# Performance work log

Hardware: AMD Instinct MI355X
Metric: run time of the kernel (lower is better)

Reference implementation:

```python
import jax, jax.numpy as jnp
import numpy as np

R_MAX = 4.0   # CUTOFF_RADIUS
N_RBF = 16    # N_BASIS
DEPTH = 2
C = 64        # pp/pi/ii node width


def setup_inputs() -> dict:
    key = jax.random.key(0)
    ks = jax.random.split(key, 16)
    N, P, B = 10000, 100000, 512
    Z = jax.random.randint(ks[0], (N,), 0, 100, dtype=jnp.int32)
    # displacement vectors; scaled so distances spread over (0, ~5) around the 4A cutoff
    pair_diff = jax.random.normal(ks[1], (P, 3), jnp.float32) * 1.5
    pair_i = jax.random.randint(ks[2], (P,), 0, N, dtype=jnp.int32)
    pair_j = jax.random.randint(ks[3], (P,), 0, N, dtype=jnp.int32)
    atom_batch = jnp.sort(jax.random.randint(ks[4], (N,), 0, B, dtype=jnp.int32))

    def w(k, shape, fan_in):
        return (jax.random.normal(k, shape, jnp.float32) / np.float32(np.sqrt(fan_in)))

    params = dict(
        embed_w=w(ks[5], (100, C), 1.0),                      # atom-type embedding
        pp_w1=w(ks[6], (DEPTH, C, C), C), pp_b1=jnp.zeros((DEPTH, C), jnp.float32),
        pp_w2=w(ks[7], (DEPTH, C, C), C), pp_b2=jnp.zeros((DEPTH, C), jnp.float32),
        pi_w1=w(ks[8], (DEPTH, 2 * C, C), 2 * C), pi_b1=jnp.zeros((DEPTH, C), jnp.float32),
        pi_w2=w(ks[9], (DEPTH, C, C * N_RBF), C), pi_b2=jnp.zeros((DEPTH, C * N_RBF), jnp.float32),
        ii_w1=w(ks[10], (DEPTH, C, C), C),                    # ii layers are bias-free
        ii_w2=w(ks[11], (DEPTH, C, 3 * C), C),                # output split 3-ways (p1/p3-scale/diff)
        pix_w=w(ks[12], (DEPTH, C, C), C),                    # equivariant (bias-free) p3 mix
        ro_w1=w(ks[13], (C, 32), C), ro_b1=jnp.zeros((32,), jnp.float32),
        ro_w2=w(ks[14], (32, 1), 32), ro_b2=jnp.zeros((1,), jnp.float32),
    )
    return dict(Z=Z, pair_diff=pair_diff, pair_i=pair_i, pair_j=pair_j,
                atom_batch=atom_batch, n_mol=B, **params)


def reference(Z, pair_diff, pair_i, pair_j, atom_batch, n_mol,
              embed_w, pp_w1, pp_b1, pp_w2, pp_b2,
              pi_w1, pi_b1, pi_w2, pi_b2,
              ii_w1, ii_w2, pix_w,
              ro_w1, ro_b1, ro_w2, ro_b2):
    N = Z.shape[0]
    dist = jnp.sqrt(jnp.sum(pair_diff * pair_diff, axis=-1) + 1e-12)   # [P]
    dhat = pair_diff / dist[:, None]                                    # unit directions [P,3]

    # Gaussian RBF basis modulated by cosine cutoff
    centers = jnp.linspace(0.0, R_MAX, N_RBF, dtype=dist.dtype)
    sigma = R_MAX / (N_RBF - 1)
    rbf = jnp.exp(-0.5 * ((dist[:, None] - centers) / sigma) ** 2)      # [P,16]
    fc = 0.5 * (jnp.cos(jnp.pi * dist / R_MAX) + 1.0) * (dist < R_MAX)
    basis = rbf * fc[:, None]                                           # [P,16]

    p1 = embed_w[Z]                                  # scalar features [N,64]
    p3 = jnp.zeros((N, 3, C), p1.dtype)              # vector features [N,3,64]

    for d in range(DEPTH):
        # pp: atomwise MLP on scalars
        h = jnp.tanh(p1 @ pp_w1[d] + pp_b1[d])
        h = jnp.tanh(h @ pp_w2[d] + pp_b2[d])
        # pi: pairwise interaction modulated by radial basis
        pij = jnp.concatenate([h[pair_i], h[pair_j]], axis=-1)          # [P,128]
        g = jnp.tanh(pij @ pi_w1[d] + pi_b1[d])
        g = jnp.tanh(g @ pi_w2[d] + pi_b2[d]).reshape(-1, C, N_RBF)     # [P,64,16]
        i1 = jnp.einsum('pcb,pb->pc', g, basis)                         # [P,64]
        # ii: bias-free pair MLP, output split into three 64-channel blocks
        ii = jnp.tanh(i1 @ ii_w1[d]) @ ii_w2[d]                         # [P,192]
        i1a, i1b, i1c = jnp.split(ii, 3, axis=-1)
        # equivariant vector messages: gathered p3_j scaled + direction term
        p3j = jnp.einsum('pxc,cd->pxd', p3[pair_j], pix_w[d])           # [P,3,64]
        i3 = p3j * i1b[:, None, :] + dhat[:, :, None] * i1c[:, None, :]
        # ip: scatter-sum messages back to atoms, residual update
        p1 = p1 + jax.ops.segment_sum(i1a, pair_i, num_segments=N)
        p3 = p3 + jax.ops.segment_sum(i3, pair_i, num_segments=N)

    # Batchwise energy readout: atomwise MLP [64,32,1], sum over atom_batch
    h = jnp.tanh(p1 @ ro_w1 + ro_b1)
    atom_e = (h @ ro_w2 + ro_b2)[:, 0]                                  # [N]
    delta_energy = jax.ops.segment_sum(atom_e, atom_batch, num_segments=n_mol)
    return delta_energy
```

## Files before the change

kernel.cpp:

```cpp
#include <hip/hip_runtime.h>
#include <hip/hip_bf16.h>

#define PI_F 3.14159265358979323846f
#define TWO_LOG2E 2.885390081777927f

#define WWIN 5
#define NBUCK 12

typedef __bf16 bf16x8 __attribute__((ext_vector_type(8)));
typedef float  f32x4  __attribute__((ext_vector_type(4)));

#define MFMA16(a, b, c) __builtin_amdgcn_mfma_f32_16x16x32_bf16((a), (b), (c), 0, 0, 0)

__device__ __forceinline__ float fast_tanh(float x) {
    float e = __builtin_amdgcn_exp2f(TWO_LOG2E * x);
    return 1.0f - 2.0f * __fdividef(1.0f, e + 1.0f);
}

__global__ void k_setup(const int* __restrict__ Z,
                        const float* __restrict__ embed_w,
                        const float* __restrict__ pair_diff,
                        const float* __restrict__ pp_w1,
                        const float* __restrict__ pp_w2,
                        const float* __restrict__ pi_w1,
                        const float* __restrict__ pi_w2,
                        const float* __restrict__ ii_w1,
                        const float* __restrict__ ii_w2,
                        const float* __restrict__ pi_b2,
                        __bf16* __restrict__ ppbf,
                        __bf16* __restrict__ w2bf,
                        __bf16* __restrict__ w3bf,
                        __bf16* __restrict__ w4bf,
                        float* __restrict__ b2t,
                        float* __restrict__ p1,
                        int* __restrict__ pb0, int* __restrict__ hist,
                        float* __restrict__ out_f,
                        int N, int P, int out_size) {
    __shared__ int h[16];
    const int t = threadIdx.x;
    const int idx = blockIdx.x * 256 + t;

    if (t < 16) h[t] = 0;
    __syncthreads();
    if (idx < P) {
        float x = pair_diff[3 * idx + 0];
        float y = pair_diff[3 * idx + 1];
        float z = pair_diff[3 * idx + 2];
        float d = sqrtf(x * x + y * y + z * z + 1e-12f);
        int b0 = -1;
        if (d < 4.0f) {
            b0 = (int)floorf(d * 3.75f + 0.5f) - 2;
            b0 = min(NBUCK - 1, max(0, b0));
            atomicAdd(&h[b0], 1);
        }
        pb0[idx] = b0;
    }
    __syncthreads();
    if (t < 16 && blockIdx.x * 256 < P) hist[blockIdx.x * 16 + t] = h[t];

    if (idx < N * 64) {
        int n = idx >> 6, c = idx & 63;
        p1[idx] = embed_w[Z[n] * 64 + c];
    }

    if (idx < out_size) out_f[idx] = 0.f;

    if (idx < 32768) {
        int k = idx & 63;
        int o = (idx >> 6) & 63;
        int d = (idx >> 12) & 1;
        int m = idx >> 13;
        float val = 0.f;
        switch (m) {
            case 0: val = pp_w1[d * 4096 + k * 64 + o]; break;
            case 1: val = pp_w2[d * 4096 + k * 64 + o]; break;
            case 2: val = pi_w1[d * 8192 + k * 64 + o]; break;
            case 3: val = pi_w1[d * 8192 + (64 + k) * 64 + o]; break;
        }
        ppbf[idx] = (__bf16)val;
    } else if (idx < 182272) {
        int j = idx - 32768;
        if (j < 131072) {
            int d = j >> 16, r = j & 65535;
            int np = r >> 6, k = r & 63;
            int b = np >> 6, c = np & 63;
            w2bf[j] = (__bf16)pi_w2[d * 65536 + k * 1024 + c * 16 + b];
        } else if (j < 139264) {
            int tt = j - 131072;
            int d = tt >> 12, r = tt & 4095;
            int n = r >> 6, k = r & 63;
            w3bf[tt] = (__bf16)ii_w1[d * 4096 + k * 64 + n];
        } else if (j < 147456) {
            int tt = j - 139264;
            int d = tt >> 12, r = tt & 4095;
            int n = r >> 6, k = r & 63;
            w4bf[tt] = (__bf16)ii_w2[d * 12288 + k * 192 + n];
        } else if (j < 149504) {
            int tt = j - 147456;
            int d = tt >> 10, r = tt & 1023;
            int b = r >> 6, c = r & 63;
            b2t[tt] = pi_b2[d * 1024 + c * 16 + b];
        }
    }
}

__global__ void k_scan(const int* __restrict__ hist, int NBL, int NB,
                       int* __restrict__ meta, int* __restrict__ bases,
                       int* __restrict__ blk_b0, int* __restrict__ aiw) {
    __shared__ int tot[NBUCK];
    __shared__ int smeta[NBUCK + 1];
    __shared__ int stile[NBUCK + 1];
    const int t = threadIdx.x;
    const int b = t >> 6, lane = t & 63;
    if (b < NBUCK) {
        int run = 0;
        for (int base = 0; base < NBL; base += 64) {
            int blk = base + lane;
            int v = (blk < NBL) ? hist[blk * 16 + b] : 0;
            int x = v;
            #pragma unroll
            for (int off = 1; off < 64; off <<= 1) {
                int y = __shfl_up(x, off);
                if (lane >= off) x += y;
            }
            if (blk < NBL) bases[b * NBL + blk] = run + x - v;
            run += __shfl(x, 63);
        }
        if (lane == 0) tot[b] = run;
    }
    __syncthreads();
    if (t == 0) {
        int s = 0, tile = 0;
        #pragma unroll
        for (int bb = 0; bb < NBUCK; ++bb) {
            smeta[bb] = s;
            stile[bb] = tile;
            int ntile = (tot[bb] + 63) >> 6;
            s += ntile << 6;
            tile += ntile;
        }
        smeta[NBUCK] = s;
        stile[NBUCK] = tile;
    }
    __syncthreads();
    if (t < NBUCK + 1) meta[t] = smeta[t];
    if (b < NBUCK) {
        int pos = smeta[b] + tot[b] + lane;
        if (pos < smeta[b + 1]) aiw[pos] = -1;
    }
    for (int tile = t; tile < NB; tile += blockDim.x) {
        int bb = -1;
        #pragma unroll
        for (int k = 0; k < NBUCK; ++k)
            if (tile >= stile[k] && tile < stile[k + 1]) bb = k;
        blk_b0[tile] = bb;
    }
}

__global__ void k_scatter(const float* __restrict__ pair_diff,
                          const int* __restrict__ pair_i, const int* __restrict__ pair_j,
                          const int* __restrict__ pb0, const int* __restrict__ meta,
                          const int* __restrict__ bases, int NBL,
                          int* __restrict__ aiw, int* __restrict__ ajw,
                          float* __restrict__ basisw, int P) {
    __shared__ int wcnt[4][NBUCK];
    int t = threadIdx.x;
    int wv = t >> 6, lane = t & 63;
    if (t < 4 * NBUCK) ((int*)wcnt)[t] = 0;
    __syncthreads();
    int p = blockIdx.x * 256 + t;
    int b0 = (p < P) ? pb0[p] : -1;
    int rank = 0;
    unsigned long long lt = (lane == 63) ? 0x7FFFFFFFFFFFFFFFull
                                         : ((1ull << lane) - 1ull);
    #pragma unroll
    for (int b = 0; b < NBUCK; ++b) {
        unsigned long long m = __ballot(b0 == b);
        if (b0 == b) {
            rank = __popcll(m & lt);
            if (rank == 0) wcnt[wv][b] = __popcll(m);
        }
    }
    __syncthreads();
    if (b0 < 0) return;
    int local = rank;
    #pragma unroll
    for (int w = 0; w < 3; ++w)
        if (w < wv) local += wcnt[w][b0];
    int pos = meta[b0] + bases[b0 * NBL + blockIdx.x] + local;
    aiw[pos] = pair_i[p];
    ajw[pos] = pair_j[p];
    float x = pair_diff[3 * p + 0];
    float y = pair_diff[3 * p + 1];
    float z = pair_diff[3 * p + 2];
    float d = sqrtf(x * x + y * y + z * z + 1e-12f);
    float fc = 0.5f * (__cosf(PI_F * d * 0.25f) + 1.0f);
    float* bw = basisw + (size_t)pos * 8;
    #pragma unroll
    for (int wb = 0; wb < WWIN; ++wb) {
        float tt = (d - (float)(b0 + wb) * (4.0f / 15.0f)) * 3.75f;
        bw[wb] = __expf(-0.5f * tt * tt) * fc;
    }
    bw[5] = 0.f;
    bw[6] = 0.f;
    bw[7] = 0.f;
}

__device__ __forceinline__ void mfma_gemm64(const __bf16 (*S)[72], const __bf16* __restrict__ W,
                                            int ll, int lg, int wv, f32x4 acc[4], float init) {
    const f32x4 i4 = {init, init, init, init};
    #pragma unroll
    for (int mt = 0; mt < 4; ++mt) acc[mt] = i4;
    #pragma unroll
    for (int kt = 0; kt < 2; ++kt) {
        bf16x8 bw = *(const bf16x8*)(W + (size_t)(wv * 16 + ll) * 64 + kt * 32 + lg * 8);
        #pragma unroll
        for (int mt = 0; mt < 4; ++mt) {
            bf16x8 af = *(const bf16x8*)&S[mt * 16 + ll][kt * 32 + lg * 8];
            acc[mt] = MFMA16(af, bw, acc[mt]);
        }
    }
}

__launch_bounds__(256)
__global__ void k_pp(const float* __restrict__ p1,
                     const __bf16* __restrict__ w1bf, const float* __restrict__ b1,
                     const __bf16* __restrict__ w2bfp, const float* __restrict__ b2,
                     const __bf16* __restrict__ wubf, const __bf16* __restrict__ wvbf,
                     const float* __restrict__ bu,
                     float* __restrict__ u, float* __restrict__ v, int N) {
    __shared__ __bf16 sA[64][72];
    __shared__ __bf16 sH[64][72];
    const int t = threadIdx.x;
    const int a0 = blockIdx.x * 64;

    {
        int r = t >> 2, q = t & 3;
        int a = a0 + r;
        int cc = q * 16;
        bf16x8 x0, x1;
        if (a < N) {
            const f32x4* pp = (const f32x4*)(p1 + (size_t)a * 64 + cc);
            f32x4 p0 = pp[0], p1v = pp[1], p2 = pp[2], p3 = pp[3];
            #pragma unroll
            for (int e = 0; e < 4; ++e) {
                x0[e]     = (__bf16)p0[e];
                x0[4 + e] = (__bf16)p1v[e];
                x1[e]     = (__bf16)p2[e];
                x1[4 + e] = (__bf16)p3[e];
            }
        } else {
            #pragma unroll
            for (int e = 0; e < 8; ++e) { x0[e] = (__bf16)0.f; x1[e] = (__bf16)0.f; }
        }
        *(bf16x8*)&sA[r][cc]     = x0;
        *(bf16x8*)&sA[r][cc + 8] = x1;
    }
    __syncthreads();

    const int l  = t & 63;
    const int wv = t >> 6;
    const int ll = l & 15;
    const int lg = l >> 4;

    f32x4 acc[4];
    mfma_gemm64(sA, w1bf, ll, lg, wv, acc, b1[wv * 16 + ll]);
    #pragma unroll
    for (int mt = 0; mt < 4; ++mt)
        #pragma unroll
        for (int r = 0; r < 4; ++r)
            sH[mt * 16 + lg * 4 + r][wv * 16 + ll] = (__bf16)fast_tanh(acc[mt][r]);
    __syncthreads();
    mfma_gemm64(sH, w2bfp, ll, lg, wv, acc, b2[wv * 16 + ll]);
    #pragma unroll
    for (int mt = 0; mt < 4; ++mt)
        #pragma unroll
        for (int r = 0; r < 4; ++r)
            sA[mt * 16 + lg * 4 + r][wv * 16 + ll] = (__bf16)fast_tanh(acc[mt][r]);
    __syncthreads();
    f32x4 accV[4];
    mfma_gemm64(sA, wubf, ll, lg, wv, acc, bu[wv * 16 + ll]);
    mfma_gemm64(sA, wvbf, ll, lg, wv, accV, 0.f);
    #pragma unroll
    for (int mt = 0; mt < 4; ++mt) {
        #pragma unroll
        for (int r = 0; r < 4; ++r) {
            int a = a0 + mt * 16 + lg * 4 + r;
            if (a < N) {
                u[(size_t)a * 64 + wv * 16 + ll] = acc[mt][r];
                v[(size_t)a * 64 + wv * 16 + ll] = accV[mt][r];
            }
        }
    }
}

__launch_bounds__(256, 5)
__global__ void k_pair(const float* __restrict__ u, const float* __restrict__ v,
                       const int* __restrict__ aiw, const int* __restrict__ ajw,
                       const float* __restrict__ basisw,
                       const __bf16* __restrict__ w2bf, const float* __restrict__ b2t,
                       const __bf16* __restrict__ w3bf, const __bf16* __restrict__ w4bf,
                       const int* __restrict__ blk_b0,
                       float* __restrict__ p1) {
    __shared__ __bf16 sGH[64][72];
    __shared__ __bf16 sI1[64][72];
    __shared__ float sB[64][12];
    __shared__ int sPi[64];

    const int b0 = blk_b0[blockIdx.x];
    if (b0 < 0) return;
    const int blk64 = blockIdx.x * 64;

    const int t  = threadIdx.x;
    const int l  = t & 63;
    const int wv = t >> 6;
    const int ll = l & 15;
    const int lg = l >> 4;

    const __bf16* abase = w2bf + ((size_t)(b0 * 64 + wv * 16 + ll) << 6) + lg * 8;
    bf16x8 a0 = *(const bf16x8*)(abase);
    bf16x8 a1 = *(const bf16x8*)(abase + 32);

    {
        int r = t >> 2, q = t & 3;
        int p = blk64 + r;
        int ai = aiw[p];
        int aj = (ai >= 0) ? ajw[p] : 0;
        if (q == 0) sPi[r] = ai;
        int cc = q * 16;
        bf16x8 g8a, g8b;
        if (ai >= 0) {
            const f32x4* up = (const f32x4*)(u + (size_t)ai * 64 + cc);
            const f32x4* vp = (const f32x4*)(v + (size_t)aj * 64 + cc);
            f32x4 u0 = up[0], u1 = up[1], u2 = up[2], u3 = up[3];
            f32x4 v0 = vp[0], v1 = vp[1], v2 = vp[2], v3 = vp[3];
            #pragma unroll
            for (int e = 0; e < 4; ++e) {
                g8a[e]     = (__bf16)fast_tanh(u0[e] + v0[e]);
                g8a[4 + e] = (__bf16)fast_tanh(u1[e] + v1[e]);
                g8b[e]     = (__bf16)fast_tanh(u2[e] + v2[e]);
                g8b[4 + e] = (__bf16)fast_tanh(u3[e] + v3[e]);
            }
        } else {
            #pragma unroll
            for (int e = 0; e < 8; ++e) { g8a[e] = (__bf16)0.f; g8b[e] = (__bf16)0.f; }
        }
        *(bf16x8*)&sGH[r][cc]     = g8a;
        *(bf16x8*)&sGH[r][cc + 8] = g8b;
        if (q < 2) {
            f32x4 b4 = {0.f, 0.f, 0.f, 0.f};
            if (ai >= 0) b4 = *(const f32x4*)(basisw + (size_t)p * 8 + q * 4);
            *(f32x4*)&sB[r][q * 4] = b4;
        }
    }
    __syncthreads();

    bf16x8 bg[4][2];
    #pragma unroll
    for (int pt = 0; pt < 4; ++pt)
        #pragma unroll
        for (int kt = 0; kt < 2; ++kt)
            bg[pt][kt] = *(const bf16x8*)&sGH[pt * 16 + ll][kt * 32 + lg * 8];

    f32x4 s[4];
    float sbsum[4];
    {
        const f32x4 z4 = {0.f, 0.f, 0.f, 0.f};
        #pragma unroll
        for (int pt = 0; pt < 4; ++pt) { s[pt] = z4; sbsum[pt] = 0.f; }
    }
    #pragma unroll 1
    for (int wb = 0; wb < WWIN; ++wb) {
        int nx = (wb < WWIN - 1) ? wb + 1 : WWIN - 1;
        bf16x8 n0 = *(const bf16x8*)(abase + nx * 4096);
        bf16x8 n1 = *(const bf16x8*)(abase + nx * 4096 + 32);

        f32x4 bias = *(const f32x4*)(b2t + (b0 + wb) * 64 + wv * 16 + lg * 4);
        f32x4 acc[4];
        #pragma unroll
        for (int pt = 0; pt < 4; ++pt) acc[pt] = bias;
        #pragma unroll
        for (int pt = 0; pt < 4; ++pt) {
            acc[pt] = MFMA16(a0, bg[pt][0], acc[pt]);
            acc[pt] = MFMA16(a1, bg[pt][1], acc[pt]);
        }
        #pragma unroll
        for (int pt = 0; pt < 4; ++pt) {
            float bas = sB[pt * 16 + ll][wb];
            sbsum[pt] += bas;
            #pragma unroll
            for (int r = 0; r < 4; ++r) {
                float e = __builtin_amdgcn_exp2f(TWO_LOG2E * acc[pt][r]);
                float rc = __fdividef(1.0f, e + 1.0f);
                s[pt][r] = fmaf(bas, rc, s[pt][r]);
            }
        }
        a0 = n0;
        a1 = n1;
    }
    #pragma unroll
    for (int pt = 0; pt < 4; ++pt) {
        __bf16 o4[4];
        #pragma unroll
        for (int r = 0; r < 4; ++r) o4[r] = (__bf16)fmaf(-2.0f, s[pt][r], sbsum[pt]);
        *(ushort2*)&sI1[pt * 16 + ll][wv * 16 + lg * 4]     = *(ushort2*)&o4[0];
        *(ushort2*)&sI1[pt * 16 + ll][wv * 16 + lg * 4 + 2] = *(ushort2*)&o4[2];
    }
    __syncthreads();

    f32x4 acc2[4];
    {
        const f32x4 z4 = {0.f, 0.f, 0.f, 0.f};
        #pragma unroll
        for (int mt = 0; mt < 4; ++mt) acc2[mt] = z4;
    }
    #pragma unroll
    for (int kt = 0; kt < 2; ++kt) {
        bf16x8 bw = *(const bf16x8*)(w3bf + (size_t)(wv * 16 + ll) * 64 + kt * 32 + lg * 8);
        #pragma unroll
        for (int mt = 0; mt < 4; ++mt) {
            bf16x8 af = *(const bf16x8*)&sI1[mt * 16 + ll][kt * 32 + lg * 8];
            acc2[mt] = MFMA16(af, bw, acc2[mt]);
        }
    }
    #pragma unroll
    for (int mt = 0; mt < 4; ++mt)
        #pragma unroll
        for (int r = 0; r < 4; ++r)
            sGH[mt * 16 + lg * 4 + r][wv * 16 + ll] = (__bf16)fast_tanh(acc2[mt][r]);
    __syncthreads();

    f32x4 acc3[4];
    {
        const f32x4 z4 = {0.f, 0.f, 0.f, 0.f};
        #pragma unroll
        for (int mt = 0; mt < 4; ++mt) acc3[mt] = z4;
    }
    #pragma unroll
    for (int kt = 0; kt < 2; ++kt) {
        bf16x8 bw = *(const bf16x8*)(w4bf + (size_t)(wv * 16 + ll) * 64 + kt * 32 + lg * 8);
        #pragma unroll
        for (int mt = 0; mt < 4; ++mt) {
            bf16x8 af = *(const bf16x8*)&sGH[mt * 16 + ll][kt * 32 + lg * 8];
            acc3[mt] = MFMA16(af, bw, acc3[mt]);
        }
    }
    #pragma unroll
    for (int mt = 0; mt < 4; ++mt) {
        #pragma unroll
        for (int r = 0; r < 4; ++r) {
            int p = mt * 16 + lg * 4 + r;
            int ai = sPi[p];
            if (ai >= 0)
                atomicAdd(p1 + (size_t)ai * 64 + wv * 16 + ll, acc3[mt][r]);
        }
    }
}

__global__ void k_readout(const float* __restrict__ p1, const float* __restrict__ rw1,
                          const float* __restrict__ rb1, const float* __restrict__ rw2,
                          const float* __restrict__ rb2, const int* __restrict__ abatch,
                          float* __restrict__ out, int N) {
    int t = threadIdx.x;
    int a = blockIdx.x * 8 + (t >> 5);
    int c = t & 31;
    if (a >= N) return;
    float acc = rb1[c];
    const float* pr = p1 + (size_t)a * 64;
    #pragma unroll
    for (int k = 0; k < 64; ++k)
        acc = fmaf(pr[k], rw1[k * 32 + c], acc);
    float e = fast_tanh(acc) * rw2[c];
    #pragma unroll
    for (int off = 16; off > 0; off >>= 1)
        e += __shfl_down(e, off, 32);
    if (c == 0) atomicAdd(&out[abatch[a]], e + rb2[0]);
}

extern "C" void kernel_launch(void* const* d_in, const int* in_sizes, int n_in,
                              void* d_out, int out_size, void* d_ws, size_t ws_size,
                              hipStream_t stream) {
    const int*   Z         = (const int*)  d_in[0];
    const float* pair_diff = (const float*)d_in[1];
    const int*   pair_i    = (const int*)  d_in[2];
    const int*   pair_j    = (const int*)  d_in[3];
    const int*   abatch    = (const int*)  d_in[4];
    const float* embed_w   = (const float*)d_in[6];
    const float* pp_w1     = (const float*)d_in[7];
    const float* pp_b1     = (const float*)d_in[8];
    const float* pp_w2     = (const float*)d_in[9];
    const float* pp_b2     = (const float*)d_in[10];
    const float* pi_w1     = (const float*)d_in[11];
    const float* pi_b1     = (const float*)d_in[12];
    const float* pi_w2     = (const float*)d_in[13];
    const float* pi_b2     = (const float*)d_in[14];
    const float* ii_w1     = (const float*)d_in[15];
    const float* ii_w2     = (const float*)d_in[16];
    const float* ro_w1     = (const float*)d_in[18];
    const float* ro_b1     = (const float*)d_in[19];
    const float* ro_w2     = (const float*)d_in[20];
    const float* ro_b2     = (const float*)d_in[21];

    const int N = in_sizes[0];
    const int P = in_sizes[2];
    const int NBL = (P + 255) / 256;
    const int NB  = (P + 63) / 64 + NBUCK + 1;
    const int Ppad = NB * 64;

    float* ws    = (float*)d_ws;
    float* p1    = ws;
    float* u     = p1 + (size_t)N * 64;
    float* v     = u + (size_t)N * 64;
    float* b2t   = v + (size_t)N * 64;
    __bf16* ppbf = (__bf16*)(b2t + 2048);
    __bf16* w2bf = ppbf + 32768;
    __bf16* w3bf = w2bf + 2 * 65536;
    __bf16* w4bf = w3bf + 2 * 4096;
    float* basisw = (float*)(w4bf + 2 * 4096);
    int*   aiw    = (int*)(basisw + (size_t)Ppad * 8);
    int*   ajw    = aiw + Ppad;
    int*   pb0    = ajw + Ppad;
    int*   meta   = pb0 + P;
    int*   hist   = meta + 16;
    int*   bases  = hist + (size_t)NBL * 16;
    int*   blk_b0 = bases + (size_t)NBUCK * NBL;

    float* out_f = (float*)d_out;

    int setup_items = N * 64;
    if (P > setup_items) setup_items = P;
    if (182272 > setup_items) setup_items = 182272;
    if (out_size > setup_items) setup_items = out_size;

    k_setup<<<(setup_items + 255) / 256, 256, 0, stream>>>(
        Z, embed_w, pair_diff, pp_w1, pp_w2, pi_w1, pi_w2, ii_w1, ii_w2, pi_b2,
        ppbf, w2bf, w3bf, w4bf, b2t, p1, pb0, hist, out_f, N, P, out_size);
    k_scan<<<1, NBUCK * 64, 0, stream>>>(hist, NBL, NB, meta, bases, blk_b0, aiw);
    k_scatter<<<NBL, 256, 0, stream>>>(pair_diff, pair_i, pair_j, pb0, meta, bases, NBL,
                                       aiw, ajw, basisw, P);

    for (int d = 0; d < 2; ++d) {
        const __bf16* w1bf_d  = ppbf + (0 * 2 + d) * 4096;
        const __bf16* w2bfp_d = ppbf + (1 * 2 + d) * 4096;
        const __bf16* wubf_d  = ppbf + (2 * 2 + d) * 4096;
        const __bf16* wvbf_d  = ppbf + (3 * 2 + d) * 4096;
        k_pp<<<(N + 63) / 64, 256, 0, stream>>>(p1, w1bf_d, pp_b1 + d * 64, w2bfp_d, pp_b2 + d * 64,
                                                wubf_d, wvbf_d, pi_b1 + d * 64, u, v, N);
        k_pair<<<NB, 256, 0, stream>>>(u, v, aiw, ajw, basisw,
                                       w2bf + (size_t)d * 65536, b2t + d * 1024,
                                       w3bf + (size_t)d * 4096, w4bf + (size_t)d * 4096,
                                       blk_b0, p1);
    }

    k_readout<<<(N + 7) / 8, 256, 0, stream>>>(p1, ro_w1, ro_b1, ro_w2, ro_b2, abatch, out_f, N);
}
```

Baseline: 130.8 us.

## Shrink pair tiles to 32 pairs with 2-wave blocks and 32-channel per-wave MFMA

Pair tiles go from 64 to 32 rows. k_pair now runs with 128 threads (two waves), and each wave covers 32 output channels as two 16-wide quads instead of 16 channels. The bucket padding in the scan and the workspace sizing move to 32-row granularity, which cuts padding waste per radial-window bucket and roughly doubles the block count. The software prefetch of the next window's weights is dropped in favour of direct loads. Each block now amortises weight loads over fewer pairs, and an extra barrier is added before sGH is overwritten.

```diff
diff --git a/kernel.cpp b/kernel.cpp
--- a/kernel.cpp
+++ b/kernel.cpp
@@ -135,8 +135,8 @@
         for (int bb = 0; bb < NBUCK; ++bb) {
             smeta[bb] = s;
             stile[bb] = tile;
-            int ntile = (tot[bb] + 63) >> 6;
-            s += ntile << 6;
+            int ntile = (tot[bb] + 31) >> 5;
+            s += ntile << 5;
             tile += ntile;
         }
         smeta[NBUCK] = s;
@@ -294,7 +294,7 @@
     }
 }
 
-__launch_bounds__(256, 5)
+__launch_bounds__(128, 6)
 __global__ void k_pair(const float* __restrict__ u, const float* __restrict__ v,
                        const int* __restrict__ aiw, const int* __restrict__ ajw,
                        const float* __restrict__ basisw,
@@ -302,14 +302,14 @@
                        const __bf16* __restrict__ w3bf, const __bf16* __restrict__ w4bf,
                        const int* __restrict__ blk_b0,
                        float* __restrict__ p1) {
-    __shared__ __bf16 sGH[64][72];
-    __shared__ __bf16 sI1[64][72];
-    __shared__ float sB[64][12];
-    __shared__ int sPi[64];
+    __shared__ __bf16 sGH[32][72];
+    __shared__ __bf16 sI1[32][72];
+    __shared__ float sB[32][12];
+    __shared__ int sPi[32];
 
     const int b0 = blk_b0[blockIdx.x];
     if (b0 < 0) return;
-    const int blk64 = blockIdx.x * 64;
+    const int blk32 = blockIdx.x * 32;
 
     const int t  = threadIdx.x;
     const int l  = t & 63;
@@ -317,13 +317,9 @@
     const int ll = l & 15;
     const int lg = l >> 4;
 
-    const __bf16* abase = w2bf + ((size_t)(b0 * 64 + wv * 16 + ll) << 6) + lg * 8;
-    bf16x8 a0 = *(const bf16x8*)(abase);
-    bf16x8 a1 = *(const bf16x8*)(abase + 32);
-
     {
         int r = t >> 2, q = t & 3;
-        int p = blk64 + r;
+        int p = blk32 + r;
         int ai = aiw[p];
         int aj = (ai >= 0) ? ajw[p] : 0;
         if (q == 0) sPi[r] = ai;
@@ -355,104 +351,138 @@
     }
     __syncthreads();
 
-    bf16x8 bg[4][2];
-    #pragma unroll
-    for (int pt = 0; pt < 4; ++pt)
+    bf16x8 bg[2][2];
+    #pragma unroll
+    for (int pt = 0; pt < 2; ++pt)
         #pragma unroll
         for (int kt = 0; kt < 2; ++kt)
             bg[pt][kt] = *(const bf16x8*)&sGH[pt * 16 + ll][kt * 32 + lg * 8];
 
-    f32x4 s[4];
-    float sbsum[4];
+    const __bf16* abase0 = w2bf + ((size_t)(b0 * 64 + wv * 32 + ll) << 6) + lg * 8;
+    const __bf16* abase1 = abase0 + (16 << 6);
+
+    f32x4 s[2][2];
+    float sbsum[2];
     {
         const f32x4 z4 = {0.f, 0.f, 0.f, 0.f};
         #pragma unroll
-        for (int pt = 0; pt < 4; ++pt) { s[pt] = z4; sbsum[pt] = 0.f; }
+        for (int qd = 0; qd < 2; ++qd)
+            #pragma unroll
+            for (int pt = 0; pt < 2; ++pt) s[qd][pt] = z4;
+        sbsum[0] = 0.f; sbsum[1] = 0.f;
     }
     #pragma unroll 1
     for (int wb = 0; wb < WWIN; ++wb) {
-        int nx = (wb < WWIN - 1) ? wb + 1 : WWIN - 1;
-        bf16x8 n0 = *(const bf16x8*)(abase + nx * 4096);
-        bf16x8 n1 = *(const bf16x8*)(abase + nx * 4096 + 32);
-
-        f32x4 bias = *(const f32x4*)(b2t + (b0 + wb) * 64 + wv * 16 + lg * 4);
-        f32x4 acc[4];
-        #pragma unroll
-        for (int pt = 0; pt < 4; ++pt) acc[pt] = bias;
-        #pragma unroll
-        for (int pt = 0; pt < 4; ++pt) {
-            acc[pt] = MFMA16(a0, bg[pt][0], acc[pt]);
-            acc[pt] = MFMA16(a1, bg[pt][1], acc[pt]);
-        }
-        #pragma unroll
-        for (int pt = 0; pt < 4; ++pt) {
+        bf16x8 a00 = *(const bf16x8*)(abase0 + wb * 4096);
+        bf16x8 a01 = *(const bf16x8*)(abase0 + wb * 4096 + 32);
+        bf16x8 a10 = *(const bf16x8*)(abase1 + wb * 4096);
+        bf16x8 a11 = *(const bf16x8*)(abase1 + wb * 4096 + 32);
+
+        #pragma unroll
+        for (int pt = 0; pt < 2; ++pt) {
             float bas = sB[pt * 16 + ll][wb];
-            sbsum[pt] += bas;
-            #pragma unroll
-            for (int r = 0; r < 4; ++r) {
-                float e = __builtin_amdgcn_exp2f(TWO_LOG2E * acc[pt][r]);
-                float rc = __fdividef(1.0f, e + 1.0f);
-                s[pt][r] = fmaf(bas, rc, s[pt][r]);
-            }
-        }
-        a0 = n0;
-        a1 = n1;
-    }
-    #pragma unroll
-    for (int pt = 0; pt < 4; ++pt) {
-        __bf16 o4[4];
-        #pragma unroll
-        for (int r = 0; r < 4; ++r) o4[r] = (__bf16)fmaf(-2.0f, s[pt][r], sbsum[pt]);
-        *(ushort2*)&sI1[pt * 16 + ll][wv * 16 + lg * 4]     = *(ushort2*)&o4[0];
-        *(ushort2*)&sI1[pt * 16 + ll][wv * 16 + lg * 4 + 2] = *(ushort2*)&o4[2];
-    }
-    __syncthreads();
-
-    f32x4 acc2[4];
+            if (pt == 0) { sbsum[0] += bas; }
+        }
+        {
+            float bas1 = sB[16 + ll][wb];
+            sbsum[1] += bas1;
+        }
+
+        #pragma unroll
+        for (int qd = 0; qd < 2; ++qd) {
+            f32x4 bias = *(const f32x4*)(b2t + (b0 + wb) * 64 + wv * 32 + qd * 16 + lg * 4);
+            bf16x8 A0 = qd ? a10 : a00;
+            bf16x8 A1 = qd ? a11 : a01;
+            #pragma unroll
+            for (int pt = 0; pt < 2; ++pt) {
+                f32x4 acc = bias;
+                acc = MFMA16(A0, bg[pt][0], acc);
+                acc = MFMA16(A1, bg[pt][1], acc);
+                float bas = sB[pt * 16 + ll][wb];
+                #pragma unroll
+                for (int r = 0; r < 4; ++r) {
+                    float e = __builtin_amdgcn_exp2f(TWO_LOG2E * acc[r]);
+                    float rc = __fdividef(1.0f, e + 1.0f);
+                    s[qd][pt][r] = fmaf(bas, rc, s[qd][pt][r]);
+                }
+            }
+        }
+    }
+    #pragma unroll
+    for (int qd = 0; qd < 2; ++qd) {
+        #pragma unroll
+        for (int pt = 0; pt < 2; ++pt) {
+            __bf16 o4[4];
+            #pragma unroll
+            for (int r = 0; r < 4; ++r) o4[r] = (__bf16)fmaf(-2.0f, s[qd][pt][r], sbsum[pt]);
+            int c0 = wv * 32 + qd * 16 + lg * 4;
+            *(ushort2*)&sI1[pt * 16 + ll][c0]     = *(ushort2*)&o4[0];
+            *(ushort2*)&sI1[pt * 16 + ll][c0 + 2] = *(ushort2*)&o4[2];
+        }
+    }
+    __syncthreads();
+
     {
+        f32x4 acc2[2][2];
         const f32x4 z4 = {0.f, 0.f, 0.f, 0.f};
         #pragma unroll
-        for (int mt = 0; mt < 4; ++mt) acc2[mt] = z4;
-    }
-    #pragma unroll
-    for (int kt = 0; kt < 2; ++kt) {
-        bf16x8 bw = *(const bf16x8*)(w3bf + (size_t)(wv * 16 + ll) * 64 + kt * 32 + lg * 8);
-        #pragma unroll
-        for (int mt = 0; mt < 4; ++mt) {
-            bf16x8 af = *(const bf16x8*)&sI1[mt * 16 + ll][kt * 32 + lg * 8];
-            acc2[mt] = MFMA16(af, bw, acc2[mt]);
-        }
-    }
-    #pragma unroll
-    for (int mt = 0; mt < 4; ++mt)
-        #pragma unroll
-        for (int r = 0; r < 4; ++r)
-            sGH[mt * 16 + lg * 4 + r][wv * 16 + ll] = (__bf16)fast_tanh(acc2[mt][r]);
-    __syncthreads();
-
-    f32x4 acc3[4];
+        for (int qd = 0; qd < 2; ++qd)
+            #pragma unroll
+            for (int mt = 0; mt < 2; ++mt) acc2[qd][mt] = z4;
+        #pragma unroll
+        for (int qd = 0; qd < 2; ++qd) {
+            #pragma unroll
+            for (int kt = 0; kt < 2; ++kt) {
+                bf16x8 bw = *(const bf16x8*)(w3bf + (size_t)(wv * 32 + qd * 16 + ll) * 64 + kt * 32 + lg * 8);
+                #pragma unroll
+                for (int mt = 0; mt < 2; ++mt) {
+                    bf16x8 af = *(const bf16x8*)&sI1[mt * 16 + ll][kt * 32 + lg * 8];
+                    acc2[qd][mt] = MFMA16(af, bw, acc2[qd][mt]);
+                }
+            }
+        }
+        __syncthreads();
+        #pragma unroll
+        for (int qd = 0; qd < 2; ++qd)
+            #pragma unroll
+            for (int mt = 0; mt < 2; ++mt)
+                #pragma unroll
+                for (int r = 0; r < 4; ++r)
+                    sGH[mt * 16 + lg * 4 + r][wv * 32 + qd * 16 + ll] = (__bf16)fast_tanh(acc2[qd][mt][r]);
+    }
+    __syncthreads();
+
     {
+        f32x4 acc3[2][2];
         const f32x4 z4 = {0.f, 0.f, 0.f, 0.f};
         #pragma unroll
-        for (int mt = 0; mt < 4; ++mt) acc3[mt] = z4;
-    }
-    #pragma unroll
-    for (int kt = 0; kt < 2; ++kt) {
-        bf16x8 bw = *(const bf16x8*)(w4bf + (size_t)(wv * 16 + ll) * 64 + kt * 32 + lg * 8);
-        #pragma unroll
-        for (int mt = 0; mt < 4; ++mt) {
-            bf16x8 af = *(const bf16x8*)&sGH[mt * 16 + ll][kt * 32 + lg * 8];
-            acc3[mt] = MFMA16(af, bw, acc3[mt]);
-        }
-    }
-    #pragma unroll
-    for (int mt = 0; mt < 4; ++mt) {
-        #pragma unroll
-        for (int r = 0; r < 4; ++r) {
-            int p = mt * 16 + lg * 4 + r;
-            int ai = sPi[p];
-            if (ai >= 0)
-                atomicAdd(p1 + (size_t)ai * 64 + wv * 16 + ll, acc3[mt][r]);
+        for (int qd = 0; qd < 2; ++qd)
+            #pragma unroll
+            for (int mt = 0; mt < 2; ++mt) acc3[qd][mt] = z4;
+        #pragma unroll
+        for (int qd = 0; qd < 2; ++qd) {
+            #pragma unroll
+            for (int kt = 0; kt < 2; ++kt) {
+                bf16x8 bw = *(const bf16x8*)(w4bf + (size_t)(wv * 32 + qd * 16 + ll) * 64 + kt * 32 + lg * 8);
+                #pragma unroll
+                for (int mt = 0; mt < 2; ++mt) {
+                    bf16x8 af = *(const bf16x8*)&sGH[mt * 16 + ll][kt * 32 + lg * 8];
+                    acc3[qd][mt] = MFMA16(af, bw, acc3[qd][mt]);
+                }
+            }
+        }
+        #pragma unroll
+        for (int qd = 0; qd < 2; ++qd) {
+            #pragma unroll
+            for (int mt = 0; mt < 2; ++mt) {
+                #pragma unroll
+                for (int r = 0; r < 4; ++r) {
+                    int p = mt * 16 + lg * 4 + r;
+                    int ai = sPi[p];
+                    if (ai >= 0)
+                        atomicAdd(p1 + (size_t)ai * 64 + wv * 32 + qd * 16 + ll, acc3[qd][mt][r]);
+                }
+            }
         }
     }
 }
@@ -504,8 +534,8 @@
     const int N = in_sizes[0];
     const int P = in_sizes[2];
     const int NBL = (P + 255) / 256;
-    const int NB  = (P + 63) / 64 + NBUCK + 1;
-    const int Ppad = NB * 64;
+    const int NB  = (P + 31) / 32 + NBUCK + 1;
+    const int Ppad = NB * 32;
 
     float* ws    = (float*)d_ws;
     float* p1    = ws;
@@ -546,7 +576,7 @@
         const __bf16* wvbf_d  = ppbf + (3 * 2 + d) * 4096;
         k_pp<<<(N + 63) / 64, 256, 0, stream>>>(p1, w1bf_d, pp_b1 + d * 64, w2bfp_d, pp_b2 + d * 64,
                                                 wubf_d, wvbf_d, pi_b1 + d * 64, u, v, N);
-        k_pair<<<NB, 256, 0, stream>>>(u, v, aiw, ajw, basisw,
+        k_pair<<<NB, 128, 0, stream>>>(u, v, aiw, ajw, basisw,
                                        w2bf + (size_t)d * 65536, b2t + d * 1024,
                                        w3bf + (size_t)d * 4096, w4bf + (size_t)d * 4096,
                                        blk_b0, p1);
```

Measured after the change: 136.9 us. 1.05x slower.
